# Kernel tuning notes

Measured on AMD Instinct MI355X. Metric: run time of the kernel, lower is better.

The kernel has to match this reference:

```python
import jax, jax.numpy as jnp
import numpy as np

NUM_POINTS = 33  # must be 2n+1
N_T = 4_194_304  # number of time samples


def setup_inputs() -> dict:
    key = jax.random.key(0)
    k1, k2 = jax.random.split(key)
    x = jax.random.uniform(k1, (N_T,), dtype=jnp.float32)  # t in [0,1]
    P = jax.random.uniform(k2, (NUM_POINTS, 5), dtype=jnp.float32)
    P = (P - P.mean()) / P.std()  # mimics initLayers normalization
    return {"x": x, "P": P}


def _basis(d):
    """d: (N,1) -> quadratic Bezier basis (N,3) = [1, d, d^2] @ B."""
    B = jnp.array([[1., 0., 0.], [-2., 2., 0.], [1., -2., 1.]], dtype=d.dtype)
    tpow = jnp.concatenate([jnp.ones_like(d), d, d * d], axis=1)  # (N,3)
    return tpow @ B


def _forward(x, P):
    num_points = P.shape[0]
    S = num_points - 2  # num_splines
    p = P[:, :2]   # (num_points, 2) means
    s = P[:, 2:]   # (num_points, 3) packed symmetric 2x2: [a, b, c] -> [[a,b],[b,c]]
    # new_sigma_mat = sigma_mat^T @ sigma_mat (sigma_mat symmetric) packed back to 3 entries
    a, b, c = s[:, 0], s[:, 1], s[:, 2]
    sig = jnp.stack([a * a + b * b, b * (a + c), b * b + c * c], axis=1)  # (num_points, 3)

    t = x[:, None]                       # (N,1)
    N = x.shape[0]
    mu0 = jnp.zeros((N, 2), x.dtype)
    sg0 = jnp.zeros((N, 3), x.dtype)
    Pn0 = p[:3]                          # (3,2)
    Sn0 = sig[:3]                        # (3,3)
    ivals = jnp.arange(S - 1, dtype=x.dtype)
    Sm1 = jnp.asarray(S - 1, x.dtype)

    def step(carry, xs):
        Pn, Sn, mu, sg = carry
        i, p_next, s_next = xs
        d = (t * Sm1 - i) * 0.5                      # (N,1)
        choice = ((d >= 0) & (d <= 0.5)).astype(x.dtype)
        cw = jnp.cos(jnp.pi * d) ** 2
        sw = jnp.sin(jnp.pi * d) ** 2
        # mean control-point recurrence
        p0 = (Pn[0] + Pn[2]) / 4 + Pn[1] / 2
        p2 = p_next
        p1 = 2.0 * (Pn[2] - (p0 + p2) / 4)
        Pn2 = jnp.stack([p0, p1, p2])                # (3,2)
        f_prev = _basis(d + 0.5) @ Pn                # (N,2)
        f_curr = _basis(d) @ Pn2
        mu = (1 - choice) * mu + choice * (cw * f_prev + sw * f_curr)
        # variance control-point recurrence
        s0 = (Sn[0] + Sn[2]) / 16 + Sn[1] / 4
        s2 = s_next
        s1 = 4.0 * (Sn[2] - (s0 + s2) / 16)
        Sn2 = jnp.stack([s0, s1, s2])                # (3,3)
        g_prev = (_basis(d + 0.5) ** 2) @ Sn         # (N,3)
        g_curr = (_basis(d) ** 2) @ Sn2
        sg = (1 - choice) * sg + choice * (cw ** 2 * g_prev + sw ** 2 * g_curr)
        return (Pn2, Sn2, mu, sg), None

    (_, _, mu, sg), _ = jax.lax.scan(step, (Pn0, Sn0, mu0, sg0), (ivals, p[3:], sig[3:]))
    return mu, sg


def reference(x, P):
    return _forward(x, P)
```

## Files before the change

kernel.cpp:

```cpp
#include <hip/hip_runtime.h>
#include <math.h>

#define QOFF 0
#define TOFF 192
#define TABSZ 472
#define PPT 4
#define NBLK 2048

__global__ __launch_bounds__(256) void yuksel_fused(
    const float* __restrict__ x, const float* __restrict__ P,
    float* __restrict__ out, int N)
{
    __shared__ float lt[TABSZ];
    const int tid = threadIdx.x;

    if (tid < 155) {
        const int e   = tid / 5;
        const int col = tid % 5;
        float v0, v1, v2;
        if (col < 2) {
            if (e == 0) {
                v0 = P[0*5+col]; v1 = P[1*5+col]; v2 = P[2*5+col];
            } else if (e == 1) {
                float p0=P[0*5+col], p1=P[1*5+col], p2=P[2*5+col], p3=P[3*5+col];
                v0 = (p0 + p2) * 0.25f + p1 * 0.5f;
                v1 = -p0*0.125f - p1*0.25f + p2*1.875f - p3*0.5f;
                v2 = p3;
            } else {
                float pe=P[e*5+col], pa=P[(e+1)*5+col], pb=P[(e+2)*5+col];
                v0 = pe;
                v1 = -pe*0.5f + 2.0f*pa - pb*0.5f;
                v2 = pb;
            }
            lt[QOFF + e*6 + col + 0] = v0;
            lt[QOFF + e*6 + col + 2] = v1;
            lt[QOFF + e*6 + col + 4] = v2;
        } else {
            const int tc = col - 2;
            auto sig = [&](int r) -> float {
                float a=P[r*5+2], b=P[r*5+3], c=P[r*5+4];
                return tc==0 ? a*a + b*b : (tc==1 ? b*(a+c) : b*b + c*c);
            };
            if (e == 0) {
                v0 = sig(0); v1 = sig(1); v2 = sig(2);
            } else if (e == 1) {
                float s0=sig(0), s1=sig(1), s2=sig(2), s3=sig(3);
                v0 = (s0 + s2) * 0.0625f + s1 * 0.25f;
                v1 = -s0*(1.0f/64.0f) - s1*0.0625f + s2*(255.0f/64.0f) - s3*0.25f;
                v2 = s3;
            } else {
                float se=sig(e), sa=sig(e+1), sb=sig(e+2);
                v0 = se;
                v1 = -se*0.25f + 4.0f*sa - sb*0.25f;
                v2 = sb;
            }
            lt[TOFF + e*9 + tc + 0] = v0;
            lt[TOFF + e*9 + tc + 3] = v1;
            lt[TOFF + e*9 + tc + 6] = v2;
        }
    }
    __syncthreads();

    const float* lQ = lt + QOFF;
    const float* lT = lt + TOFF;

    const long long stride = (long long)gridDim.x * 256 * PPT;
    for (long long j0 = ((long long)blockIdx.x * 256 + tid) * PPT; j0 < N; j0 += stride) {
        float4 xv = *reinterpret_cast<const float4*>(x + j0);
        float xs[PPT] = { xv.x, xv.y, xv.z, xv.w };
        float mu[2*PPT], sg[3*PPT];

#pragma unroll
        for (int q = 0; q < PPT; ++q) {
            float u  = xs[q] * 30.0f;
            float fi = floorf(u);
            fi = fminf(fmaxf(fi, 0.0f), 29.0f);
            int   i  = (int)fi;
            float d  = (u - fi) * 0.5f;
            float e  = d + 0.5f;

            float omd = 1.0f - d;
            float bc0 = omd * omd, bc1 = 2.0f * d * omd, bc2 = d * d;
            float ome = 1.0f - e;
            float bp0 = ome * ome, bp1 = 2.0f * e * ome, bp2 = e * e;

            float cpi = cospif(d);
            float cw  = cpi * cpi;
            float sw  = 1.0f - cw;
            float cw2 = cw * cw, sw2 = sw * sw;

            const float* Qi = lQ + i * 6;
            const float* Ti = lT + i * 9;

            float fpx = bp0*Qi[0] + bp1*Qi[2] + bp2*Qi[4];
            float fpy = bp0*Qi[1] + bp1*Qi[3] + bp2*Qi[5];
            float fcx = bc0*Qi[6] + bc1*Qi[8] + bc2*Qi[10];
            float fcy = bc0*Qi[7] + bc1*Qi[9] + bc2*Qi[11];
            mu[2*q+0] = cw*fpx + sw*fcx;
            mu[2*q+1] = cw*fpy + sw*fcy;

            float a0 = bp0*bp0, a1 = bp1*bp1, a2 = bp2*bp2;
            float c0 = bc0*bc0, c1 = bc1*bc1, c2 = bc2*bc2;
            float gp0 = a0*Ti[0] + a1*Ti[3] + a2*Ti[6];
            float gp1 = a0*Ti[1] + a1*Ti[4] + a2*Ti[7];
            float gp2 = a0*Ti[2] + a1*Ti[5] + a2*Ti[8];
            float gc0 = c0*Ti[9]  + c1*Ti[12] + c2*Ti[15];
            float gc1 = c0*Ti[10] + c1*Ti[13] + c2*Ti[16];
            float gc2 = c0*Ti[11] + c1*Ti[14] + c2*Ti[17];
            sg[3*q+0] = cw2*gp0 + sw2*gc0;
            sg[3*q+1] = cw2*gp1 + sw2*gc1;
            sg[3*q+2] = cw2*gp2 + sw2*gc2;
        }

        float4* muOut = reinterpret_cast<float4*>(out + 2*j0);
        muOut[0] = make_float4(mu[0], mu[1], mu[2], mu[3]);
        muOut[1] = make_float4(mu[4], mu[5], mu[6], mu[7]);
        float4* sgOut = reinterpret_cast<float4*>(out + (size_t)2*N + 3*j0);
        sgOut[0] = make_float4(sg[0], sg[1], sg[2],  sg[3]);
        sgOut[1] = make_float4(sg[4], sg[5], sg[6],  sg[7]);
        sgOut[2] = make_float4(sg[8], sg[9], sg[10], sg[11]);
    }
}

extern "C" void kernel_launch(void* const* d_in, const int* in_sizes, int n_in,
                              void* d_out, int out_size, void* d_ws, size_t ws_size,
                              hipStream_t stream) {
    const float* x = (const float*)d_in[0];
    const float* P = (const float*)d_in[1];
    float* out = (float*)d_out;
    int N = in_sizes[0];

    const int threads = 256;
    const int per_block = threads * PPT;
    long long ntiles = (N + per_block - 1) / per_block;
    int blocks = (int)(ntiles < NBLK ? ntiles : NBLK);
    yuksel_fused<<<blocks, threads, 0, stream>>>(x, P, out, N);
}
```

Measured before the change: 30.33 us.

## Fold spline recurrence into 4-point weights over a compact control-point table

Replaces the precomputed per-segment 3-point mean and variance control tables with a 5x33 table of raw means and sigma entries. Each sample now computes four combined weights per output, so every output becomes a single 4-term dot product over neighbouring table entries. cospif squared is replaced by 0.5+0.5*__builtin_amdgcn_cosf(d), the hardware cosine that takes its argument in revolutions. The aim is fewer ALU instructions and fewer LDS loads per sample, at the cost of slightly different floating-point rounding and reliance on the approximate hardware cosine.

```diff
diff --git a/kernel.cpp b/kernel.cpp
--- a/kernel.cpp
+++ b/kernel.cpp
@@ -1,9 +1,7 @@
 #include <hip/hip_runtime.h>
 #include <math.h>
 
-#define QOFF 0
-#define TOFF 192
-#define TABSZ 472
+#define NENT 33
 #define PPT 4
 #define NBLK 2048
 
@@ -11,58 +9,30 @@
     const float* __restrict__ x, const float* __restrict__ P,
     float* __restrict__ out, int N)
 {
-    __shared__ float lt[TABSZ];
+    __shared__ float ltab[5][NENT];
     const int tid = threadIdx.x;
 
-    if (tid < 155) {
-        const int e   = tid / 5;
-        const int col = tid % 5;
-        float v0, v1, v2;
-        if (col < 2) {
-            if (e == 0) {
-                v0 = P[0*5+col]; v1 = P[1*5+col]; v2 = P[2*5+col];
-            } else if (e == 1) {
-                float p0=P[0*5+col], p1=P[1*5+col], p2=P[2*5+col], p3=P[3*5+col];
-                v0 = (p0 + p2) * 0.25f + p1 * 0.5f;
-                v1 = -p0*0.125f - p1*0.25f + p2*1.875f - p3*0.5f;
-                v2 = p3;
-            } else {
-                float pe=P[e*5+col], pa=P[(e+1)*5+col], pb=P[(e+2)*5+col];
-                v0 = pe;
-                v1 = -pe*0.5f + 2.0f*pa - pb*0.5f;
-                v2 = pb;
+    if (tid < NENT) {
+        const int e = tid;
+        float vals[5];
+        if (e == 1) {
+            float r0[5], r1[5], r2[5];
+            for (int r = 0; r < 3; ++r) {
+                float* dst = r==0 ? r0 : (r==1 ? r1 : r2);
+                float a = P[r*5+2], b = P[r*5+3], c = P[r*5+4];
+                dst[0] = P[r*5+0]; dst[1] = P[r*5+1];
+                dst[2] = a*a + b*b; dst[3] = b*(a+c); dst[4] = b*b + c*c;
             }
-            lt[QOFF + e*6 + col + 0] = v0;
-            lt[QOFF + e*6 + col + 2] = v1;
-            lt[QOFF + e*6 + col + 4] = v2;
+            for (int k = 0; k < 2; ++k) vals[k] = (r0[k]+r2[k])*0.25f   + r1[k]*0.5f;
+            for (int k = 2; k < 5; ++k) vals[k] = (r0[k]+r2[k])*0.0625f + r1[k]*0.25f;
         } else {
-            const int tc = col - 2;
-            auto sig = [&](int r) -> float {
-                float a=P[r*5+2], b=P[r*5+3], c=P[r*5+4];
-                return tc==0 ? a*a + b*b : (tc==1 ? b*(a+c) : b*b + c*c);
-            };
-            if (e == 0) {
-                v0 = sig(0); v1 = sig(1); v2 = sig(2);
-            } else if (e == 1) {
-                float s0=sig(0), s1=sig(1), s2=sig(2), s3=sig(3);
-                v0 = (s0 + s2) * 0.0625f + s1 * 0.25f;
-                v1 = -s0*(1.0f/64.0f) - s1*0.0625f + s2*(255.0f/64.0f) - s3*0.25f;
-                v2 = s3;
-            } else {
-                float se=sig(e), sa=sig(e+1), sb=sig(e+2);
-                v0 = se;
-                v1 = -se*0.25f + 4.0f*sa - sb*0.25f;
-                v2 = sb;
-            }
-            lt[TOFF + e*9 + tc + 0] = v0;
-            lt[TOFF + e*9 + tc + 3] = v1;
-            lt[TOFF + e*9 + tc + 6] = v2;
+            float a = P[e*5+2], b = P[e*5+3], c = P[e*5+4];
+            vals[0] = P[e*5+0]; vals[1] = P[e*5+1];
+            vals[2] = a*a + b*b; vals[3] = b*(a+c); vals[4] = b*b + c*c;
         }
+        for (int k = 0; k < 5; ++k) ltab[k][e] = vals[k];
     }
     __syncthreads();
-
-    const float* lQ = lt + QOFF;
-    const float* lT = lt + TOFF;
 
     const long long stride = (long long)gridDim.x * 256 * PPT;
     for (long long j0 = ((long long)blockIdx.x * 256 + tid) * PPT; j0 < N; j0 += stride) {
@@ -73,43 +43,41 @@
 #pragma unroll
         for (int q = 0; q < PPT; ++q) {
             float u  = xs[q] * 30.0f;
-            float fi = floorf(u);
-            fi = fminf(fmaxf(fi, 0.0f), 29.0f);
+            float fi = fminf(fmaxf(floorf(u), 0.0f), 29.0f);
             int   i  = (int)fi;
             float d  = (u - fi) * 0.5f;
             float e  = d + 0.5f;
 
-            float omd = 1.0f - d;
-            float bc0 = omd * omd, bc1 = 2.0f * d * omd, bc2 = d * d;
-            float ome = 1.0f - e;
-            float bp0 = ome * ome, bp1 = 2.0f * e * ome, bp2 = e * e;
+            float omd = 1.0f - d, ome = 1.0f - e;
+            float bc0 = omd*omd, bc1 = 2.0f*d*omd, bc2 = d*d;
+            float bp0 = ome*ome, bp1 = 2.0f*e*ome, bp2 = e*e;
 
-            float cpi = cospif(d);
-            float cw  = cpi * cpi;
+            float cw  = 0.5f + 0.5f*__builtin_amdgcn_cosf(d);
             float sw  = 1.0f - cw;
-            float cw2 = cw * cw, sw2 = sw * sw;
+            float cw2 = cw*cw, sw2 = sw*sw;
 
-            const float* Qi = lQ + i * 6;
-            const float* Ti = lT + i * 9;
-
-            float fpx = bp0*Qi[0] + bp1*Qi[2] + bp2*Qi[4];
-            float fpy = bp0*Qi[1] + bp1*Qi[3] + bp2*Qi[5];
-            float fcx = bc0*Qi[6] + bc1*Qi[8] + bc2*Qi[10];
-            float fcy = bc0*Qi[7] + bc1*Qi[9] + bc2*Qi[11];
-            mu[2*q+0] = cw*fpx + sw*fcx;
-            mu[2*q+1] = cw*fpy + sw*fcy;
-
+            float w0 = cw*(bp0 - 0.5f*bp1);
+            float w1 = 2.0f*cw*bp1 + sw*(bc0 - 0.5f*bc1);
+            float w2 = cw*(bp2 - 0.5f*bp1) + 2.0f*sw*bc1;
+            float w3 = sw*(bc2 - 0.5f*bc1);
             float a0 = bp0*bp0, a1 = bp1*bp1, a2 = bp2*bp2;
             float c0 = bc0*bc0, c1 = bc1*bc1, c2 = bc2*bc2;
-            float gp0 = a0*Ti[0] + a1*Ti[3] + a2*Ti[6];
-            float gp1 = a0*Ti[1] + a1*Ti[4] + a2*Ti[7];
-            float gp2 = a0*Ti[2] + a1*Ti[5] + a2*Ti[8];
-            float gc0 = c0*Ti[9]  + c1*Ti[12] + c2*Ti[15];
-            float gc1 = c0*Ti[10] + c1*Ti[13] + c2*Ti[16];
-            float gc2 = c0*Ti[11] + c1*Ti[14] + c2*Ti[17];
-            sg[3*q+0] = cw2*gp0 + sw2*gc0;
-            sg[3*q+1] = cw2*gp1 + sw2*gc1;
-            sg[3*q+2] = cw2*gp2 + sw2*gc2;
+            float v0 = cw2*(a0 - 0.25f*a1);
+            float v1 = 4.0f*cw2*a1 + sw2*(c0 - 0.25f*c1);
+            float v2 = cw2*(a2 - 0.25f*a1) + 4.0f*sw2*c1;
+            float v3 = sw2*(c2 - 0.25f*c1);
+
+            float px0 = ltab[0][i],   px1 = ltab[0][i+1], px2 = ltab[0][i+2], px3 = ltab[0][i+3];
+            float py0 = ltab[1][i],   py1 = ltab[1][i+1], py2 = ltab[1][i+2], py3 = ltab[1][i+3];
+            float s00 = ltab[2][i],   s01 = ltab[2][i+1], s02 = ltab[2][i+2], s03 = ltab[2][i+3];
+            float s10 = ltab[3][i],   s11 = ltab[3][i+1], s12 = ltab[3][i+2], s13 = ltab[3][i+3];
+            float s20 = ltab[4][i],   s21 = ltab[4][i+1], s22 = ltab[4][i+2], s23 = ltab[4][i+3];
+
+            mu[2*q+0] = w0*px0 + w1*px1 + w2*px2 + w3*px3;
+            mu[2*q+1] = w0*py0 + w1*py1 + w2*py2 + w3*py3;
+            sg[3*q+0] = v0*s00 + v1*s01 + v2*s02 + v3*s03;
+            sg[3*q+1] = v0*s10 + v1*s11 + v2*s12 + v3*s13;
+            sg[3*q+2] = v0*s20 + v1*s21 + v2*s22 + v3*s23;
         }
 
         float4* muOut = reinterpret_cast<float4*>(out + 2*j0);
```

Measured after the change: 26.28 us. -13.3%, faster.
